# Optimization experiments

Measured on AMD Instinct MI355X. Metric: run time of the kernel, lower is better.

The kernel has to match this reference:

```python
import jax, jax.numpy as jnp
import numpy as np

B, L, D = 4, 2048, 1024
H, HD = 16, 64
N = 2048  # total number of sets across the batch
TOPK = 8


def setup_inputs() -> dict:
    key = jax.random.key(0)
    ks = jax.random.split(key, 10)
    s = 0.02
    # ragged segment pointers: roughly equal segments with jitter, min length >= TOPK
    rng = np.random.default_rng(0)
    base = N // B
    jit = rng.integers(-base // 4, base // 4, size=B)
    lens = np.maximum(base + jit, TOPK + 1)
    lens = (lens * (N / lens.sum())).astype(np.int64)
    lens[-1] = N - lens[:-1].sum()
    q_ptrs = jnp.asarray(np.concatenate([[0], np.cumsum(lens)]), dtype=jnp.int64)
    return {
        "token_states": jax.random.normal(ks[0], (B, L, D), jnp.float32),
        "Z_sets": jax.random.normal(ks[1], (N, H, HD), jnp.float32),
        "desc_q": jax.random.normal(ks[2], (N, D), jnp.float32),
        "q_ptrs": q_ptrs,
        "Wg_w": jax.random.normal(ks[3], (D, D), jnp.float32) * s,
        "Wg_b": jnp.zeros((D,), jnp.float32),
        "Wd_w": jax.random.normal(ks[4], (D, D), jnp.float32) * s,
        "Wd_b": jnp.zeros((D,), jnp.float32),
        "out_w": jax.random.normal(ks[5], (D, D), jnp.float32) * s,
        "out_b": jnp.zeros((D,), jnp.float32),
    }


def reference(token_states, Z_sets, desc_q, q_ptrs, Wg_w, Wg_b, Wd_w, Wd_b, out_w, out_b):
    Bs, Ls, Ds = token_states.shape
    Ns = desc_q.shape[0]
    S = Ns  # static pad width (upper bound on max segment length)
    starts = q_ptrs[:-1]                       # [B]
    lengths = q_ptrs[1:] - starts              # [B]
    pos = jnp.arange(S)
    idx = jnp.clip(starts[:, None] + pos[None, :], 0, Ns - 1)   # [B,S]
    valid = pos[None, :] < lengths[:, None]                      # [B,S] bool
    desc_pad = jnp.where(valid[..., None], desc_q[idx], 0.0)     # [B,S,D]
    z_pad = jnp.where(valid[..., None, None], Z_sets[idx], 0.0)  # [B,S,H,HD]

    Tproj = token_states @ Wg_w.T + Wg_b                         # [B,L,D]
    Dproj = desc_pad @ Wd_w.T + Wd_b                             # [B,S,D]
    logits = jnp.einsum('bld,bsd->bls', Tproj, Dproj)            # [B,L,S]
    logits = jnp.where(valid[:, None, :], logits, -jnp.inf)

    if TOPK > 0 and S > TOPK:
        vals, tidx = jax.lax.top_k(logits, TOPK)                 # [B,L,K]
        bidx = jnp.arange(Bs)[:, None, None]
        lidx = jnp.arange(Ls)[None, :, None]
        tmp = jnp.full_like(logits, -jnp.inf)
        tmp = tmp.at[bidx, lidx, tidx].set(vals)
        gates = jax.nn.softmax(tmp, axis=-1)
    else:
        gates = jax.nn.softmax(logits, axis=-1)

    mix = jnp.einsum('bls,bshd->blhd', gates, z_pad)             # [B,L,H,HD]
    return mix.reshape(Bs, Ls, Ds) @ out_w.T + out_b
```

## Files before the change

### kernel.cpp

```cpp
#include <hip/hip_runtime.h>
#include <hip/hip_bf16.h>
#include <math.h>

#define BQ    4
#define LQ    2048
#define D_DIM 1024
#define NQ    2048
#define SMAX  1024
#define TOPK  8

typedef __attribute__((ext_vector_type(8))) short          short8;
typedef __attribute__((ext_vector_type(8))) _Float16       half8;
typedef __attribute__((ext_vector_type(4))) float          f32x4;
typedef __attribute__((ext_vector_type(8))) unsigned short ushort8;
typedef __attribute__((ext_vector_type(4))) unsigned short ushort4v;

typedef __attribute__((address_space(3))) void as3_void;
typedef __attribute__((address_space(1))) void as1_void;

__device__ __forceinline__ void gload_lds16(const void* g, void* l) {
    __builtin_amdgcn_global_load_lds((const as1_void*)g, (as3_void*)l, 16, 0, 0);
}

__device__ __forceinline__ unsigned short f2bf(float f) {
    __hip_bfloat16 h = __float2bfloat16(f);
    return *reinterpret_cast<unsigned short*>(&h);
}
__device__ __forceinline__ float bf2f(unsigned short u) {
    unsigned int w = (unsigned int)u << 16;
    return *reinterpret_cast<float*>(&w);
}
__device__ __forceinline__ unsigned short f2h(float f) {
    _Float16 h = (_Float16)f;
    return *reinterpret_cast<unsigned short*>(&h);
}
__device__ __forceinline__ float h2f(unsigned short u) {
    _Float16 h = *reinterpret_cast<_Float16*>(&u);
    return (float)h;
}

__device__ __forceinline__ int swz(int r) { return (r ^ (r >> 2)) & 3; }

#define WAIT_VM0   asm volatile("s_waitcnt vmcnt(0)" ::: "memory")
#define WAIT_VM3   asm volatile("s_waitcnt vmcnt(3)" ::: "memory")
#define WAIT_VM4   asm volatile("s_waitcnt vmcnt(4)" ::: "memory")
#define WAIT_VM6   asm volatile("s_waitcnt vmcnt(6)" ::: "memory")
#define WAIT_LGKM0 asm volatile("s_waitcnt lgkmcnt(0)" ::: "memory")

__global__ __launch_bounds__(256) void k_cvt_all(
    const float* __restrict__ token_states, const float* __restrict__ desc_q,
    const float* __restrict__ Wg_w, const float* __restrict__ Wd_w,
    const float* __restrict__ out_w, const float* __restrict__ Z_sets,
    const int* __restrict__ q_raw,
    unsigned short* __restrict__ tokenH, unsigned short* __restrict__ tokenL,
    unsigned short* __restrict__ descH,  unsigned short* __restrict__ descL,
    unsigned short* __restrict__ wgh,    unsigned short* __restrict__ wdh,
    unsigned short* __restrict__ owb,    unsigned short* __restrict__ Zb,
    int* __restrict__ qp)
{
    const int blk = blockIdx.x;
    if (blk == 0 && threadIdx.x == 0) {
        bool is64 = (q_raw[1] == 0);
        for (int i = 0; i <= BQ; ++i)
            qp[i] = is64 ? q_raw[2 * i] : q_raw[i];
    }

    const float* in; unsigned short *hi, *lo = nullptr; int local; bool fp16m = true;
    if (blk < 4096)      { in = token_states; hi = tokenH; lo = tokenL; local = blk; }
    else if (blk < 5120) { in = desc_q; hi = descH; lo = descL; local = blk - 4096; }
    else if (blk < 5632) { in = Wg_w;   hi = wgh;   local = blk - 5120; }
    else if (blk < 6144) { in = Wd_w;   hi = wdh;   local = blk - 5632; }
    else if (blk < 6656) { in = out_w;  hi = owb;   local = blk - 6144; fp16m = false; }
    else                 { in = Z_sets; hi = Zb;    local = blk - 6656; fp16m = false; }

    int i = (local * 256 + threadIdx.x) * 8;
    float4 v0 = *reinterpret_cast<const float4*>(in + i);
    float4 v1 = *reinterpret_cast<const float4*>(in + i + 4);
    float x[8] = {v0.x, v0.y, v0.z, v0.w, v1.x, v1.y, v1.z, v1.w};
    ushort8 h8, l8;
#pragma unroll
    for (int k = 0; k < 8; ++k) {
        if (fp16m) {
            unsigned short h = f2h(x[k]);
            h8[k] = h;
            l8[k] = f2h(x[k] - h2f(h));
        } else {
            h8[k] = f2bf(x[k]);
        }
    }
    *reinterpret_cast<ushort8*>(hi + i) = h8;
    if (lo) *reinterpret_cast<ushort8*>(lo + i) = l8;
}

__global__ __launch_bounds__(256) void k_gemm_2p(
    const unsigned short* __restrict__ Ah, const unsigned short* __restrict__ Al,
    const unsigned short* __restrict__ Wh,
    const float* __restrict__ bias, unsigned short* __restrict__ C,
    int M, int N, int K)
{
    __shared__ __align__(16) char lds[2 * 24576];

    const int nbx = gridDim.x;
    const int total = nbx * gridDim.y;
    const int d = blockIdx.x + nbx * blockIdx.y;
    const int logical = (d & 7) * (total >> 3) + (d >> 3);
    const int bcol = (logical % nbx) * 128;
    const int brow = (logical / nbx) * 128;

    const int tid = threadIdx.x;
    const int ln  = tid & 63;
    const int wid = tid >> 6;
    const int wm  = wid >> 1, wn = wid & 1;
    const int fr  = ln & 15, fs = ln >> 4;
    const int srow = tid >> 2;
    const int sslt = tid & 3;

    const int kk0 = (sslt ^ swz(srow)) << 3;
    const size_t offA0 = (size_t)(brow + srow) * K + kk0;
    const size_t offW0 = (size_t)(bcol + srow) * K + kk0;

    auto stage = [&](char* base, int k0) {
        gload_lds16(Ah + offA0 + k0,          base + wid * 1024);
        gload_lds16(Ah + offA0 + 64 * K + k0, base + 4096 + wid * 1024);
        gload_lds16(Al + offA0 + k0,          base + 8192 + wid * 1024);
        gload_lds16(Al + offA0 + 64 * K + k0, base + 12288 + wid * 1024);
        gload_lds16(Wh + offW0 + k0,          base + 16384 + wid * 1024);
        gload_lds16(Wh + offW0 + 64 * K + k0, base + 20480 + wid * 1024);
    };

    f32x4 acc[4][4] = {};

    stage(lds, 0);
    stage(lds + 24576, 32);

    const int NT = K / 32;
    for (int t = 0; t < NT; ++t) {
        if (t < NT - 1) { WAIT_VM6; } else { WAIT_VM0; }
        __builtin_amdgcn_s_barrier();

        char* base = lds + (t & 1) * 24576;
        half8 ahf[4], alf[4], bhf[4];
#pragma unroll
        for (int mi = 0; mi < 4; ++mi) {
            int r = wm * 64 + mi * 16 + fr;
            int o = r * 64 + ((fs ^ swz(r)) << 4);
            ahf[mi] = *reinterpret_cast<const half8*>(base + o);
            alf[mi] = *reinterpret_cast<const half8*>(base + 8192 + o);
        }
#pragma unroll
        for (int ni = 0; ni < 4; ++ni) {
            int c = wn * 64 + ni * 16 + fr;
            int o = c * 64 + ((fs ^ swz(c)) << 4);
            bhf[ni] = *reinterpret_cast<const half8*>(base + 16384 + o);
        }
        __builtin_amdgcn_s_setprio(1);
#pragma unroll
        for (int mi = 0; mi < 4; ++mi)
#pragma unroll
            for (int ni = 0; ni < 4; ++ni)
                acc[mi][ni] = __builtin_amdgcn_mfma_f32_16x16x32_f16(
                    ahf[mi], bhf[ni], acc[mi][ni], 0, 0, 0);
#pragma unroll
        for (int mi = 0; mi < 4; ++mi)
#pragma unroll
            for (int ni = 0; ni < 4; ++ni)
                acc[mi][ni] = __builtin_amdgcn_mfma_f32_16x16x32_f16(
                    alf[mi], bhf[ni], acc[mi][ni], 0, 0, 0);
        __builtin_amdgcn_s_setprio(0);

        WAIT_LGKM0;
        __builtin_amdgcn_s_barrier();
        if (t + 2 < NT) stage(base, (t + 2) * 32);
    }

    float bv[4];
#pragma unroll
    for (int ni = 0; ni < 4; ++ni)
        bv[ni] = bias[bcol + wn * 64 + ni * 16 + fr];

#pragma unroll
    for (int mi = 0; mi < 4; ++mi) {
#pragma unroll
        for (int reg = 0; reg < 4; ++reg) {
            int row = brow + wm * 64 + mi * 16 + fs * 4 + reg;
#pragma unroll
            for (int ni = 0; ni < 4; ++ni) {
                int col = bcol + wn * 64 + ni * 16 + fr;
                C[(size_t)row * N + col] = f2h(acc[mi][ni][reg] + bv[ni]);
            }
        }
    }
}

__global__ __launch_bounds__(256) void k_dzw(
    const unsigned short* __restrict__ descH, const unsigned short* __restrict__ descL,
    const unsigned short* __restrict__ wdh,
    const float* __restrict__ Wd_b, unsigned short* __restrict__ Dproj16,
    const unsigned short* __restrict__ Zb, const unsigned short* __restrict__ owb,
    unsigned short* __restrict__ ZWb)
{
    constexpr int K = D_DIM, N = D_DIM;
    __shared__ __align__(16) char lds[2 * 24576];

    const int d = blockIdx.x;
    const int sub = d >> 1;
    const int bcol = (sub & 7) * 128;
    const int brow = (sub >> 3) * 128;

    const int tid = threadIdx.x;
    const int ln  = tid & 63;
    const int wid = tid >> 6;
    const int wm  = wid >> 1, wn = wid & 1;
    const int fr  = ln & 15, fs = ln >> 4;
    const int srow = tid >> 2;
    const int sslt = tid & 3;

    const int kk0 = (sslt ^ swz(srow)) << 3;
    const size_t offA0 = (size_t)(brow + srow) * K + kk0;
    const size_t offW0 = (size_t)(bcol + srow) * K + kk0;

    if ((d & 1) == 0) {
        auto stage = [&](char* base, int k0) {
            gload_lds16(descH + offA0 + k0,          base + wid * 1024);
            gload_lds16(descH + offA0 + 64 * K + k0, base + 4096 + wid * 1024);
            gload_lds16(descL + offA0 + k0,          base + 8192 + wid * 1024);
            gload_lds16(descL + offA0 + 64 * K + k0, base + 12288 + wid * 1024);
            gload_lds16(wdh + offW0 + k0,            base + 16384 + wid * 1024);
            gload_lds16(wdh + offW0 + 64 * K + k0,   base + 20480 + wid * 1024);
        };

        f32x4 acc[4][4] = {};
        stage(lds, 0);
        stage(lds + 24576, 32);

        const int NT = K / 32;
        for (int t = 0; t < NT; ++t) {
            if (t < NT - 1) { WAIT_VM6; } else { WAIT_VM0; }
            __builtin_amdgcn_s_barrier();

            char* base = lds + (t & 1) * 24576;
            half8 ahf[4], alf[4], bhf[4];
#pragma unroll
            for (int mi = 0; mi < 4; ++mi) {
                int r = wm * 64 + mi * 16 + fr;
                int o = r * 64 + ((fs ^ swz(r)) << 4);
                ahf[mi] = *reinterpret_cast<const half8*>(base + o);
                alf[mi] = *reinterpret_cast<const half8*>(base + 8192 + o);
            }
#pragma unroll
            for (int ni = 0; ni < 4; ++ni) {
                int c = wn * 64 + ni * 16 + fr;
                int o = c * 64 + ((fs ^ swz(c)) << 4);
                bhf[ni] = *reinterpret_cast<const half8*>(base + 16384 + o);
            }
            __builtin_amdgcn_s_setprio(1);
#pragma unroll
            for (int mi = 0; mi < 4; ++mi)
#pragma unroll
                for (int ni = 0; ni < 4; ++ni)
                    acc[mi][ni] = __builtin_amdgcn_mfma_f32_16x16x32_f16(
                        ahf[mi], bhf[ni], acc[mi][ni], 0, 0, 0);
#pragma unroll
            for (int mi = 0; mi < 4; ++mi)
#pragma unroll
                for (int ni = 0; ni < 4; ++ni)
                    acc[mi][ni] = __builtin_amdgcn_mfma_f32_16x16x32_f16(
                        alf[mi], bhf[ni], acc[mi][ni], 0, 0, 0);
            __builtin_amdgcn_s_setprio(0);

            WAIT_LGKM0;
            __builtin_amdgcn_s_barrier();
            if (t + 2 < NT) stage(base, (t + 2) * 32);
        }

        float bv[4];
#pragma unroll
        for (int ni = 0; ni < 4; ++ni)
            bv[ni] = Wd_b[bcol + wn * 64 + ni * 16 + fr];

#pragma unroll
        for (int mi = 0; mi < 4; ++mi) {
#pragma unroll
            for (int reg = 0; reg < 4; ++reg) {
                int row = brow + wm * 64 + mi * 16 + fs * 4 + reg;
#pragma unroll
                for (int ni = 0; ni < 4; ++ni) {
                    int col = bcol + wn * 64 + ni * 16 + fr;
                    Dproj16[(size_t)row * N + col] = f2h(acc[mi][ni][reg] + bv[ni]);
                }
            }
        }
    } else {
        auto stage = [&](char* base, int k0) {
            gload_lds16(Zb + offA0 + k0,           base + wid * 1024);
            gload_lds16(Zb + offA0 + 64 * K + k0,  base + 4096 + wid * 1024);
            gload_lds16(owb + offW0 + k0,          base + 8192 + wid * 1024);
            gload_lds16(owb + offW0 + 64 * K + k0, base + 12288 + wid * 1024);
        };

        f32x4 acc[4][4] = {};
        stage(lds, 0);
        stage(lds + 24576, 32);

        const int NT = K / 32;
        for (int t = 0; t < NT; ++t) {
            if (t < NT - 1) { WAIT_VM4; } else { WAIT_VM0; }
            __builtin_amdgcn_s_barrier();

            char* base = lds + (t & 1) * 24576;
            short8 a[4], bfr[4];
#pragma unroll
            for (int mi = 0; mi < 4; ++mi) {
                int r = wm * 64 + mi * 16 + fr;
                a[mi] = *reinterpret_cast<const short8*>(base + r * 64 + ((fs ^ swz(r)) << 4));
            }
#pragma unroll
            for (int ni = 0; ni < 4; ++ni) {
                int c = wn * 64 + ni * 16 + fr;
                bfr[ni] = *reinterpret_cast<const short8*>(base + 8192 + c * 64 + ((fs ^ swz(c)) << 4));
            }
            __builtin_amdgcn_s_setprio(1);
#pragma unroll
            for (int mi = 0; mi < 4; ++mi)
#pragma unroll
                for (int ni = 0; ni < 4; ++ni)
                    acc[mi][ni] = __builtin_amdgcn_mfma_f32_16x16x32_bf16(
                        a[mi], bfr[ni], acc[mi][ni], 0, 0, 0);
            __builtin_amdgcn_s_setprio(0);

            WAIT_LGKM0;
            __builtin_amdgcn_s_barrier();
            if (t + 2 < NT) stage(base, (t + 2) * 32);
        }

#pragma unroll
        for (int mi = 0; mi < 4; ++mi) {
#pragma unroll
            for (int reg = 0; reg < 4; ++reg) {
                int row = brow + wm * 64 + mi * 16 + fs * 4 + reg;
#pragma unroll
                for (int ni = 0; ni < 4; ++ni) {
                    int col = bcol + wn * 64 + ni * 16 + fr;
                    ZWb[(size_t)row * N + col] = f2bf(acc[mi][ni][reg]);
                }
            }
        }
    }
}

__global__ __launch_bounds__(256) void k_logits_fp16(
    const unsigned short* __restrict__ T16, const unsigned short* __restrict__ D16,
    const int* __restrict__ qp, float* __restrict__ logits)
{
    const int d = blockIdx.x + 16 * (blockIdx.y + 16 * blockIdx.z);
    const int logical = (d & 7) * 128 + (d >> 3);
    const int b    = logical >> 8;
    const int brow = ((logical >> 4) & 15) * 128;
    const int bcol = (logical & 15) * 64;

    const int start = qp[b], len = qp[b + 1] - start;
    if (bcol >= len) return;

    __shared__ __align__(16) char lds[2 * 12288];

    const int tid = threadIdx.x;
    const int ln  = tid & 63;
    const int wid = tid >> 6;
    const int fr  = ln & 15, fs = ln >> 4;
    const int srow = tid >> 2;
    const int sslt = tid & 3;

    const int kka = (sslt ^ swz(srow)) << 3;
    const size_t offA0 = ((size_t)b * LQ + brow + srow) * D_DIM + kka;
    int wr = start + bcol + srow; if (wr > NQ - 1) wr = NQ - 1;
    const size_t offW0 = (size_t)wr * D_DIM + kka;

    auto stage = [&](char* base, int k0) {
        gload_lds16(T16 + offA0 + k0,              base + wid * 1024);
        gload_lds16(T16 + offA0 + 64 * D_DIM + k0, base + 4096 + wid * 1024);
        gload_lds16(D16 + offW0 + k0,              base + 8192 + wid * 1024);
    };

    f32x4 acc[2][4] = {};

    stage(lds, 0);
    stage(lds + 12288, 32);

    const int NT = D_DIM / 32;
    for (int t = 0; t < NT; ++t) {
        if (t < NT - 1) { WAIT_VM3; } else { WAIT_VM0; }
        __builtin_amdgcn_s_barrier();

        char* base = lds + (t & 1) * 12288;
        half8 a[2], bf[4];
#pragma unroll
        for (int mi = 0; mi < 2; ++mi) {
            int r = wid * 32 + mi * 16 + fr;
            a[mi] = *reinterpret_cast<const half8*>(base + r * 64 + ((fs ^ swz(r)) << 4));
        }
#pragma unroll
        for (int ni = 0; ni < 4; ++ni) {
            int c = ni * 16 + fr;
            bf[ni] = *reinterpret_cast<const half8*>(base + 8192 + c * 64 + ((fs ^ swz(c)) << 4));
        }
        __builtin_amdgcn_s_setprio(1);
#pragma unroll
        for (int mi = 0; mi < 2; ++mi)
#pragma unroll
            for (int ni = 0; ni < 4; ++ni)
                acc[mi][ni] = __builtin_amdgcn_mfma_f32_16x16x32_f16(
                    a[mi], bf[ni], acc[mi][ni], 0, 0, 0);
        __builtin_amdgcn_s_setprio(0);

        WAIT_LGKM0;
        __builtin_amdgcn_s_barrier();
        if (t + 2 < NT) stage(base, (t + 2) * 32);
    }

#pragma unroll
    for (int mi = 0; mi < 2; ++mi) {
#pragma unroll
        for (int reg = 0; reg < 4; ++reg) {
            size_t row = (size_t)b * LQ + brow + wid * 32 + mi * 16 + fs * 4 + reg;
#pragma unroll
            for (int ni = 0; ni < 4; ++ni) {
                int col = bcol + ni * 16 + fr;
                logits[row * SMAX + col] = acc[mi][ni][reg];
            }
        }
    }
}

__global__ __launch_bounds__(256) void k_topk_out(
    const float* __restrict__ logits, const unsigned short* __restrict__ ZW,
    const float* __restrict__ out_b, const int* __restrict__ qp,
    float* __restrict__ out)
{
    const int ln  = threadIdx.x & 63;
    const int row = blockIdx.x * 4 + (threadIdx.x >> 6);
    const int b   = row >> 11;
    const int start = qp[b], len = qp[b + 1] - start;

    const float* lrow = logits + (size_t)row * SMAX;

    float v[16];
#pragma unroll
    for (int c = 0; c < 4; ++c) {
        float4 q = reinterpret_cast<const float4*>(lrow)[c * 64 + ln];
        int s0 = c * 256 + ln * 4;
        v[c * 4 + 0] = (s0 + 0 < len) ? q.x : -INFINITY;
        v[c * 4 + 1] = (s0 + 1 < len) ? q.y : -INFINITY;
        v[c * 4 + 2] = (s0 + 2 < len) ? q.z : -INFINITY;
        v[c * 4 + 3] = (s0 + 3 < len) ? q.w : -INFINITY;
    }

    float wv[TOPK]; int wi[TOPK];
#pragma unroll
    for (int it = 0; it < TOPK; ++it) {
        float bvv = v[0]; int bj = 0;
#pragma unroll
        for (int j = 1; j < 16; ++j)
            if (v[j] > bvv) { bvv = v[j]; bj = j; }
        int gidx = (bj >> 2) * 256 + ln * 4 + (bj & 3);
        float cv = bvv; int ci = gidx;
#pragma unroll
        for (int off = 32; off > 0; off >>= 1) {
            float ov = __shfl_xor(cv, off);
            int   oi = __shfl_xor(ci, off);
            if (ov > cv || (ov == cv && oi < ci)) { cv = ov; ci = oi; }
        }
        wv[it] = cv; wi[it] = ci;
#pragma unroll
        for (int j = 0; j < 16; ++j) {
            int sj = (j >> 2) * 256 + ln * 4 + (j & 3);
            if (sj == ci) v[j] = -INFINITY;
        }
    }

    float m = wv[0], denom = 0.f;
    float g[TOPK];
#pragma unroll
    for (int k = 0; k < TOPK; ++k) { g[k] = expf(wv[k] - m); denom += g[k]; }
    float inv = 1.f / denom;

    float4 acc[4];
#pragma unroll
    for (int c = 0; c < 4; ++c)
        acc[c] = reinterpret_cast<const float4*>(out_b)[c * 64 + ln];

#pragma unroll
    for (int k = 0; k < TOPK; ++k) {
        int si = wi[k] >= 0 ? wi[k] : 0;
        const ushort4v* zr = reinterpret_cast<const ushort4v*>(
            ZW + (size_t)(start + si) * D_DIM);
        float wgt = g[k] * inv;
#pragma unroll
        for (int c = 0; c < 4; ++c) {
            ushort4v z = zr[c * 64 + ln];
            acc[c].x = fmaf(wgt, bf2f(z[0]), acc[c].x);
            acc[c].y = fmaf(wgt, bf2f(z[1]), acc[c].y);
            acc[c].z = fmaf(wgt, bf2f(z[2]), acc[c].z);
            acc[c].w = fmaf(wgt, bf2f(z[3]), acc[c].w);
        }
    }
    float* orow = out + (size_t)row * D_DIM;
#pragma unroll
    for (int c = 0; c < 4; ++c)
        reinterpret_cast<float4*>(orow)[c * 64 + ln] = acc[c];
}

extern "C" void kernel_launch(void* const* d_in, const int* in_sizes, int n_in,
                              void* d_out, int out_size, void* d_ws, size_t ws_size,
                              hipStream_t stream) {
    const float* token_states = (const float*)d_in[0];
    const float* Z_sets       = (const float*)d_in[1];
    const float* desc_q       = (const float*)d_in[2];
    const int*   q_raw        = (const int*)d_in[3];
    const float* Wg_w  = (const float*)d_in[4];
    const float* Wg_b  = (const float*)d_in[5];
    const float* Wd_w  = (const float*)d_in[6];
    const float* Wd_b  = (const float*)d_in[7];
    const float* out_w = (const float*)d_in[8];
    const float* out_b = (const float*)d_in[9];
    float* out = (float*)d_out;

    const size_t NTOK = (size_t)BQ * LQ * D_DIM;
    const size_t NDES = (size_t)NQ * D_DIM;
    const size_t NW   = (size_t)D_DIM * D_DIM;

    char* ws = (char*)d_ws;
    int* qp = (int*)ws;
    unsigned short* tokenH  = (unsigned short*)(ws + 256);
    unsigned short* tokenL  = tokenH + NTOK;
    unsigned short* descH   = tokenL + NTOK;
    unsigned short* descL   = descH + NDES;
    unsigned short* wgh     = descL + NDES;
    unsigned short* wdh     = wgh + NW;
    unsigned short* owb     = wdh + NW;
    unsigned short* Zb      = owb + NW;
    unsigned short* Tproj16 = Zb + NDES;
    unsigned short* Dproj16 = Tproj16 + NTOK;
    unsigned short* ZWb     = Dproj16 + NDES;
    float* logit = (float*)tokenH;

    k_cvt_all<<<7680, 256, 0, stream>>>(
        token_states, desc_q, Wg_w, Wd_w, out_w, Z_sets, q_raw,
        tokenH, tokenL, descH, descL, wgh, wdh, owb, Zb, qp);

    k_gemm_2p<<<dim3(8, 64), 256, 0, stream>>>(
        tokenH, tokenL, wgh, Wg_b, Tproj16, BQ * LQ, D_DIM, D_DIM);

    k_dzw<<<256, 256, 0, stream>>>(
        descH, descL, wdh, Wd_b, Dproj16, Zb, owb, ZWb);

    k_logits_fp16<<<dim3(SMAX / 64, LQ / 128, BQ), 256, 0, stream>>>(
        Tproj16, Dproj16, qp, logit);

    k_topk_out<<<(BQ * LQ) / 4, 256, 0, stream>>>(logit, ZWb, out_b, qp, out);
}
```

Baseline: 139.1 us.

## Reassociate gate logits: fold Wg into descriptor projection instead of token projection

```diff
diff --git a/kernel.cpp b/kernel.cpp
--- a/kernel.cpp
+++ b/kernel.cpp
@@ -42,21 +42,19 @@
 __device__ __forceinline__ int swz(int r) { return (r ^ (r >> 2)) & 3; }
 
 #define WAIT_VM0   asm volatile("s_waitcnt vmcnt(0)" ::: "memory")
-#define WAIT_VM3   asm volatile("s_waitcnt vmcnt(3)" ::: "memory")
 #define WAIT_VM4   asm volatile("s_waitcnt vmcnt(4)" ::: "memory")
+#define WAIT_VM5   asm volatile("s_waitcnt vmcnt(5)" ::: "memory")
 #define WAIT_VM6   asm volatile("s_waitcnt vmcnt(6)" ::: "memory")
 #define WAIT_LGKM0 asm volatile("s_waitcnt lgkmcnt(0)" ::: "memory")
 
 __global__ __launch_bounds__(256) void k_cvt_all(
     const float* __restrict__ token_states, const float* __restrict__ desc_q,
-    const float* __restrict__ Wg_w, const float* __restrict__ Wd_w,
-    const float* __restrict__ out_w, const float* __restrict__ Z_sets,
-    const int* __restrict__ q_raw,
+    const float* __restrict__ Wd_w, const float* __restrict__ out_w,
+    const float* __restrict__ Z_sets, const int* __restrict__ q_raw,
     unsigned short* __restrict__ tokenH, unsigned short* __restrict__ tokenL,
     unsigned short* __restrict__ descH,  unsigned short* __restrict__ descL,
-    unsigned short* __restrict__ wgh,    unsigned short* __restrict__ wdh,
-    unsigned short* __restrict__ owb,    unsigned short* __restrict__ Zb,
-    int* __restrict__ qp)
+    unsigned short* __restrict__ wdh,    unsigned short* __restrict__ owb,
+    unsigned short* __restrict__ Zb,     int* __restrict__ qp)
 {
     const int blk = blockIdx.x;
     if (blk == 0 && threadIdx.x == 0) {
@@ -68,10 +66,9 @@
     const float* in; unsigned short *hi, *lo = nullptr; int local; bool fp16m = true;
     if (blk < 4096)      { in = token_states; hi = tokenH; lo = tokenL; local = blk; }
     else if (blk < 5120) { in = desc_q; hi = descH; lo = descL; local = blk - 4096; }
-    else if (blk < 5632) { in = Wg_w;   hi = wgh;   local = blk - 5120; }
-    else if (blk < 6144) { in = Wd_w;   hi = wdh;   local = blk - 5632; }
-    else if (blk < 6656) { in = out_w;  hi = owb;   local = blk - 6144; fp16m = false; }
-    else                 { in = Z_sets; hi = Zb;    local = blk - 6656; fp16m = false; }
+    else if (blk < 5632) { in = Wd_w;   hi = wdh;   local = blk - 5120; }
+    else if (blk < 6144) { in = out_w;  hi = owb;   local = blk - 5632; fp16m = false; }
+    else                 { in = Z_sets; hi = Zb;    local = blk - 6144; fp16m = false; }
 
     int i = (local * 256 + threadIdx.x) * 8;
     float4 v0 = *reinterpret_cast<const float4*>(in + i);
@@ -92,103 +89,25 @@
     if (lo) *reinterpret_cast<ushort8*>(lo + i) = l8;
 }
 
-__global__ __launch_bounds__(256) void k_gemm_2p(
-    const unsigned short* __restrict__ Ah, const unsigned short* __restrict__ Al,
-    const unsigned short* __restrict__ Wh,
-    const float* __restrict__ bias, unsigned short* __restrict__ C,
-    int M, int N, int K)
+__global__ __launch_bounds__(256) void k_wgt(
+    const float* __restrict__ Wg, unsigned short* __restrict__ wgT)
 {
-    __shared__ __align__(16) char lds[2 * 24576];
-
-    const int nbx = gridDim.x;
-    const int total = nbx * gridDim.y;
-    const int d = blockIdx.x + nbx * blockIdx.y;
-    const int logical = (d & 7) * (total >> 3) + (d >> 3);
-    const int bcol = (logical % nbx) * 128;
-    const int brow = (logical / nbx) * 128;
-
+    __shared__ float t[64][65];
     const int tid = threadIdx.x;
-    const int ln  = tid & 63;
-    const int wid = tid >> 6;
-    const int wm  = wid >> 1, wn = wid & 1;
-    const int fr  = ln & 15, fs = ln >> 4;
-    const int srow = tid >> 2;
-    const int sslt = tid & 3;
-
-    const int kk0 = (sslt ^ swz(srow)) << 3;
-    const size_t offA0 = (size_t)(brow + srow) * K + kk0;
-    const size_t offW0 = (size_t)(bcol + srow) * K + kk0;
-
-    auto stage = [&](char* base, int k0) {
-        gload_lds16(Ah + offA0 + k0,          base + wid * 1024);
-        gload_lds16(Ah + offA0 + 64 * K + k0, base + 4096 + wid * 1024);
-        gload_lds16(Al + offA0 + k0,          base + 8192 + wid * 1024);
-        gload_lds16(Al + offA0 + 64 * K + k0, base + 12288 + wid * 1024);
-        gload_lds16(Wh + offW0 + k0,          base + 16384 + wid * 1024);
-        gload_lds16(Wh + offW0 + 64 * K + k0, base + 20480 + wid * 1024);
-    };
-
-    f32x4 acc[4][4] = {};
-
-    stage(lds, 0);
-    stage(lds + 24576, 32);
-
-    const int NT = K / 32;
-    for (int t = 0; t < NT; ++t) {
-        if (t < NT - 1) { WAIT_VM6; } else { WAIT_VM0; }
-        __builtin_amdgcn_s_barrier();
-
-        char* base = lds + (t & 1) * 24576;
-        half8 ahf[4], alf[4], bhf[4];
-#pragma unroll
-        for (int mi = 0; mi < 4; ++mi) {
-            int r = wm * 64 + mi * 16 + fr;
-            int o = r * 64 + ((fs ^ swz(r)) << 4);
-            ahf[mi] = *reinterpret_cast<const half8*>(base + o);
-            alf[mi] = *reinterpret_cast<const half8*>(base + 8192 + o);
-        }
-#pragma unroll
-        for (int ni = 0; ni < 4; ++ni) {
-            int c = wn * 64 + ni * 16 + fr;
-            int o = c * 64 + ((fs ^ swz(c)) << 4);
-            bhf[ni] = *reinterpret_cast<const half8*>(base + 16384 + o);
-        }
-        __builtin_amdgcn_s_setprio(1);
-#pragma unroll
-        for (int mi = 0; mi < 4; ++mi)
-#pragma unroll
-            for (int ni = 0; ni < 4; ++ni)
-                acc[mi][ni] = __builtin_amdgcn_mfma_f32_16x16x32_f16(
-                    ahf[mi], bhf[ni], acc[mi][ni], 0, 0, 0);
-#pragma unroll
-        for (int mi = 0; mi < 4; ++mi)
-#pragma unroll
-            for (int ni = 0; ni < 4; ++ni)
-                acc[mi][ni] = __builtin_amdgcn_mfma_f32_16x16x32_f16(
-                    alf[mi], bhf[ni], acc[mi][ni], 0, 0, 0);
-        __builtin_amdgcn_s_setprio(0);
-
-        WAIT_LGKM0;
-        __builtin_amdgcn_s_barrier();
-        if (t + 2 < NT) stage(base, (t + 2) * 32);
-    }
-
-    float bv[4];
-#pragma unroll
-    for (int ni = 0; ni < 4; ++ni)
-        bv[ni] = bias[bcol + wn * 64 + ni * 16 + fr];
-
-#pragma unroll
-    for (int mi = 0; mi < 4; ++mi) {
-#pragma unroll
-        for (int reg = 0; reg < 4; ++reg) {
-            int row = brow + wm * 64 + mi * 16 + fs * 4 + reg;
-#pragma unroll
-            for (int ni = 0; ni < 4; ++ni) {
-                int col = bcol + wn * 64 + ni * 16 + fr;
-                C[(size_t)row * N + col] = f2h(acc[mi][ni][reg] + bv[ni]);
-            }
-        }
+    const int j0 = (blockIdx.x & 15) * 64;
+    const int d0 = (blockIdx.x >> 4) * 64;
+#pragma unroll
+    for (int i = 0; i < 16; ++i) {
+        int r = i * 4 + (tid >> 6);
+        int c = tid & 63;
+        t[r][c] = Wg[(size_t)(d0 + r) * D_DIM + j0 + c];
+    }
+    __syncthreads();
+#pragma unroll
+    for (int i = 0; i < 16; ++i) {
+        int jj = i * 4 + (tid >> 6);
+        int dd = tid & 63;
+        wgT[(size_t)(j0 + jj) * D_DIM + d0 + dd] = f2h(t[dd][jj]);
     }
 }
 
@@ -308,7 +227,7 @@
             __builtin_amdgcn_s_barrier();
 
             char* base = lds + (t & 1) * 24576;
-            short8 a[4], bfr[4];
+            short8 a[4], b[4];
 #pragma unroll
             for (int mi = 0; mi < 4; ++mi) {
                 int r = wm * 64 + mi * 16 + fr;
@@ -317,7 +236,7 @@
 #pragma unroll
             for (int ni = 0; ni < 4; ++ni) {
                 int c = wn * 64 + ni * 16 + fr;
-                bfr[ni] = *reinterpret_cast<const short8*>(base + 8192 + c * 64 + ((fs ^ swz(c)) << 4));
+                b[ni] = *reinterpret_cast<const short8*>(base + 8192 + c * 64 + ((fs ^ swz(c)) << 4));
             }
             __builtin_amdgcn_s_setprio(1);
 #pragma unroll
@@ -325,7 +244,7 @@
 #pragma unroll
                 for (int ni = 0; ni < 4; ++ni)
                     acc[mi][ni] = __builtin_amdgcn_mfma_f32_16x16x32_bf16(
-                        a[mi], bfr[ni], acc[mi][ni], 0, 0, 0);
+                        a[mi], b[ni], acc[mi][ni], 0, 0, 0);
             __builtin_amdgcn_s_setprio(0);
 
             WAIT_LGKM0;
@@ -348,8 +267,112 @@
     }
 }
 
-__global__ __launch_bounds__(256) void k_logits_fp16(
-    const unsigned short* __restrict__ T16, const unsigned short* __restrict__ D16,
+__global__ __launch_bounds__(256) void k_g(
+    const unsigned short* __restrict__ A, const unsigned short* __restrict__ W,
+    unsigned short* __restrict__ C, int M, int N, int K)
+{
+    __shared__ __align__(16) char lds[2 * 16384];
+
+    const int nbx = gridDim.x;
+    const int total = nbx * gridDim.y;
+    const int d = blockIdx.x + nbx * blockIdx.y;
+    const int logical = (d & 7) * (total >> 3) + (d >> 3);
+    const int bcol = (logical % nbx) * 128;
+    const int brow = (logical / nbx) * 128;
+
+    const int tid = threadIdx.x;
+    const int ln  = tid & 63;
+    const int wid = tid >> 6;
+    const int wm  = wid >> 1, wn = wid & 1;
+    const int fr  = ln & 15, fs = ln >> 4;
+    const int srow = tid >> 2;
+    const int sslt = tid & 3;
+
+    const int kk0 = (sslt ^ swz(srow)) << 3;
+    const size_t offA0 = (size_t)(brow + srow) * K + kk0;
+    const size_t offW0 = (size_t)(bcol + srow) * K + kk0;
+
+    auto stage = [&](char* base, int k0) {
+        gload_lds16(A + offA0 + k0,          base + wid * 1024);
+        gload_lds16(A + offA0 + 64 * K + k0, base + 4096 + wid * 1024);
+        gload_lds16(W + offW0 + k0,          base + 8192 + wid * 1024);
+        gload_lds16(W + offW0 + 64 * K + k0, base + 12288 + wid * 1024);
+    };
+
+    f32x4 acc[4][4] = {};
+
+    stage(lds, 0);
+    stage(lds + 16384, 32);
+
+    const int NT = K / 32;
+    for (int t = 0; t < NT; ++t) {
+        if (t < NT - 1) { WAIT_VM4; } else { WAIT_VM0; }
+        __builtin_amdgcn_s_barrier();
+
+        char* base = lds + (t & 1) * 16384;
+        half8 a[4], b[4];
+#pragma unroll
+        for (int mi = 0; mi < 4; ++mi) {
+            int r = wm * 64 + mi * 16 + fr;
+            a[mi] = *reinterpret_cast<const half8*>(base + r * 64 + ((fs ^ swz(r)) << 4));
+        }
+#pragma unroll
+        for (int ni = 0; ni < 4; ++ni) {
+            int c = wn * 64 + ni * 16 + fr;
+            b[ni] = *reinterpret_cast<const half8*>(base + 8192 + c * 64 + ((fs ^ swz(c)) << 4));
+        }
+        __builtin_amdgcn_s_setprio(1);
+#pragma unroll
+        for (int mi = 0; mi < 4; ++mi)
+#pragma unroll
+            for (int ni = 0; ni < 4; ++ni)
+                acc[mi][ni] = __builtin_amdgcn_mfma_f32_16x16x32_f16(
+                    a[mi], b[ni], acc[mi][ni], 0, 0, 0);
+        __builtin_amdgcn_s_setprio(0);
+
+        WAIT_LGKM0;
+        __builtin_amdgcn_s_barrier();
+        if (t + 2 < NT) stage(base, (t + 2) * 32);
+    }
+
+#pragma unroll
+    for (int mi = 0; mi < 4; ++mi) {
+#pragma unroll
+        for (int reg = 0; reg < 4; ++reg) {
+            int row = brow + wm * 64 + mi * 16 + fs * 4 + reg;
+#pragma unroll
+            for (int ni = 0; ni < 4; ++ni) {
+                int col = bcol + wn * 64 + ni * 16 + fr;
+                C[(size_t)row * N + col] = f2h(acc[mi][ni][reg]);
+            }
+        }
+    }
+}
+
+__global__ __launch_bounds__(256) void k_cvec(
+    const unsigned short* __restrict__ Dproj16, const float* __restrict__ bg,
+    float* __restrict__ c)
+{
+    const int row = blockIdx.x * 4 + (threadIdx.x >> 6);
+    const int ln  = threadIdx.x & 63;
+    const unsigned short* dr = Dproj16 + (size_t)row * D_DIM + ln * 16;
+    float s = 0.f;
+#pragma unroll
+    for (int h = 0; h < 2; ++h) {
+        ushort8 v = *reinterpret_cast<const ushort8*>(dr + h * 8);
+#pragma unroll
+        for (int j = 0; j < 8; ++j)
+            s = fmaf(bg[ln * 16 + h * 8 + j], h2f(v[j]), s);
+    }
+#pragma unroll
+    for (int off = 32; off > 0; off >>= 1)
+        s += __shfl_xor(s, off);
+    if (ln == 0) c[row] = s;
+}
+
+__global__ __launch_bounds__(256) void k_logits_2p(
+    const unsigned short* __restrict__ TH, const unsigned short* __restrict__ TL,
+    const unsigned short* __restrict__ G16, const float* __restrict__ cvec,
     const int* __restrict__ qp, float* __restrict__ logits)
 {
     const int d = blockIdx.x + 16 * (blockIdx.y + 16 * blockIdx.z);
@@ -361,7 +384,7 @@
     const int start = qp[b], len = qp[b + 1] - start;
     if (bcol >= len) return;
 
-    __shared__ __align__(16) char lds[2 * 12288];
+    __shared__ __align__(16) char lds[2 * 20480];
 
     const int tid = threadIdx.x;
     const int ln  = tid & 63;
@@ -376,32 +399,36 @@
     const size_t offW0 = (size_t)wr * D_DIM + kka;
 
     auto stage = [&](char* base, int k0) {
-        gload_lds16(T16 + offA0 + k0,              base + wid * 1024);
-        gload_lds16(T16 + offA0 + 64 * D_DIM + k0, base + 4096 + wid * 1024);
-        gload_lds16(D16 + offW0 + k0,              base + 8192 + wid * 1024);
+        gload_lds16(TH + offA0 + k0,              base + wid * 1024);
+        gload_lds16(TH + offA0 + 64 * D_DIM + k0, base + 4096 + wid * 1024);
+        gload_lds16(TL + offA0 + k0,              base + 8192 + wid * 1024);
+        gload_lds16(TL + offA0 + 64 * D_DIM + k0, base + 12288 + wid * 1024);
+        gload_lds16(G16 + offW0 + k0,             base + 16384 + wid * 1024);
     };
 
     f32x4 acc[2][4] = {};
 
     stage(lds, 0);
-    stage(lds + 12288, 32);
+    stage(lds + 20480, 32);
 
     const int NT = D_DIM / 32;
     for (int t = 0; t < NT; ++t) {
-        if (t < NT - 1) { WAIT_VM3; } else { WAIT_VM0; }
+        if (t < NT - 1) { WAIT_VM5; } else { WAIT_VM0; }
         __builtin_amdgcn_s_barrier();
 
-        char* base = lds + (t & 1) * 12288;
-        half8 a[2], bf[4];
+        char* base = lds + (t & 1) * 20480;
+        half8 ah[2], al[2], bf[4];
 #pragma unroll
         for (int mi = 0; mi < 2; ++mi) {
             int r = wid * 32 + mi * 16 + fr;
-            a[mi] = *reinterpret_cast<const half8*>(base + r * 64 + ((fs ^ swz(r)) << 4));
+            int o = r * 64 + ((fs ^ swz(r)) << 4);
+            ah[mi] = *reinterpret_cast<const half8*>(base + o);
+            al[mi] = *reinterpret_cast<const half8*>(base + 8192 + o);
         }
 #pragma unroll
         for (int ni = 0; ni < 4; ++ni) {
             int c = ni * 16 + fr;
-            bf[ni] = *reinterpret_cast<const half8*>(base + 8192 + c * 64 + ((fs ^ swz(c)) << 4));
+            bf[ni] = *reinterpret_cast<const half8*>(base + 16384 + c * 64 + ((fs ^ swz(c)) << 4));
         }
         __builtin_amdgcn_s_setprio(1);
 #pragma unroll
@@ -409,7 +436,13 @@
 #pragma unroll
             for (int ni = 0; ni < 4; ++ni)
                 acc[mi][ni] = __builtin_amdgcn_mfma_f32_16x16x32_f16(
-                    a[mi], bf[ni], acc[mi][ni], 0, 0, 0);
+                    ah[mi], bf[ni], acc[mi][ni], 0, 0, 0);
+#pragma unroll
+        for (int mi = 0; mi < 2; ++mi)
+#pragma unroll
+            for (int ni = 0; ni < 4; ++ni)
+                acc[mi][ni] = __builtin_amdgcn_mfma_f32_16x16x32_f16(
+                    al[mi], bf[ni], acc[mi][ni], 0, 0, 0);
         __builtin_amdgcn_s_setprio(0);
 
         WAIT_LGKM0;
@@ -417,6 +450,14 @@
         if (t + 2 < NT) stage(base, (t + 2) * 32);
     }
 
+    float cv[4];
+#pragma unroll
+    for (int ni = 0; ni < 4; ++ni) {
+        int ci = start + bcol + ni * 16 + fr;
+        if (ci > NQ - 1) ci = NQ - 1;
+        cv[ni] = cvec[ci];
+    }
+
 #pragma unroll
     for (int mi = 0; mi < 2; ++mi) {
 #pragma unroll
@@ -425,7 +466,7 @@
 #pragma unroll
             for (int ni = 0; ni < 4; ++ni) {
                 int col = bcol + ni * 16 + fr;
-                logits[row * SMAX + col] = acc[mi][ni][reg];
+                logits[row * SMAX + col] = acc[mi][ni][reg] + cv[ni];
             }
         }
     }
@@ -534,27 +575,31 @@
     unsigned short* tokenL  = tokenH + NTOK;
     unsigned short* descH   = tokenL + NTOK;
     unsigned short* descL   = descH + NDES;
-    unsigned short* wgh     = descL + NDES;
-    unsigned short* wdh     = wgh + NW;
-    unsigned short* owb     = wdh + NW;
+    unsigned short* wdh     = descL + NDES;
+    unsigned short* wgT     = wdh + NW;
+    unsigned short* owb     = wgT + NW;
     unsigned short* Zb      = owb + NW;
-    unsigned short* Tproj16 = Zb + NDES;
-    unsigned short* Dproj16 = Tproj16 + NTOK;
+    unsigned short* Dproj16 = Zb + NDES;
     unsigned short* ZWb     = Dproj16 + NDES;
-    float* logit = (float*)tokenH;
-
-    k_cvt_all<<<7680, 256, 0, stream>>>(
-        token_states, desc_q, Wg_w, Wd_w, out_w, Z_sets, q_raw,
-        tokenH, tokenL, descH, descL, wgh, wdh, owb, Zb, qp);
-
-    k_gemm_2p<<<dim3(8, 64), 256, 0, stream>>>(
-        tokenH, tokenL, wgh, Wg_b, Tproj16, BQ * LQ, D_DIM, D_DIM);
+    unsigned short* G16     = ZWb + NDES;
+    float* cvec             = (float*)(G16 + NDES);
+    float* logit            = cvec + 2048;
+
+    k_cvt_all<<<7168, 256, 0, stream>>>(
+        token_states, desc_q, Wd_w, out_w, Z_sets, q_raw,
+        tokenH, tokenL, descH, descL, wdh, owb, Zb, qp);
+
+    k_wgt<<<256, 256, 0, stream>>>(Wg_w, wgT);
 
     k_dzw<<<256, 256, 0, stream>>>(
         descH, descL, wdh, Wd_b, Dproj16, Zb, owb, ZWb);
 
-    k_logits_fp16<<<dim3(SMAX / 64, LQ / 128, BQ), 256, 0, stream>>>(
-        Tproj16, Dproj16, qp, logit);
+    k_g<<<dim3(8, 16), 256, 0, stream>>>(Dproj16, wgT, G16, NQ, D_DIM, D_DIM);
+
+    k_cvec<<<512, 256, 0, stream>>>(Dproj16, Wg_b, cvec);
+
+    k_logits_2p<<<dim3(SMAX / 64, LQ / 128, BQ), 256, 0, stream>>>(
+        tokenH, tokenL, G16, cvec, qp, logit);
 
     k_topk_out<<<(BQ * LQ) / 4, 256, 0, stream>>>(logit, ZWb, out_b, qp, out);
 }
```

Result: no change. 136.7 us (-1.8%).
